# Optimization experiments

Hardware: AMD Instinct MI355X
Metric: run time of the kernel (lower is better)

Reference implementation:

```python
import jax, jax.numpy as jnp
import numpy as np

NUM_TRACKS = [5313, 1643, 128, 0]
MAX_TRACKS = max(NUM_TRACKS)
EMBED_DIM = 1536
LN_EPS = 1e-5


def setup_inputs() -> dict:
    key = jax.random.key(0)
    ks = jax.random.split(key, 8)
    B, S, D = 4, 896, EMBED_DIM
    inp = {
        "x": jax.random.normal(ks[0], (B, S, D), dtype=jnp.float32),
        "head_idx": jax.random.randint(ks[1], (B,), 0, 4, dtype=jnp.int64) if jax.config.jax_enable_x64 else jax.random.randint(ks[1], (B,), 0, 4).astype(jnp.int32),
    }
    for i, n in enumerate([5313, 1643, 128]):
        inp[f"gamma{i}"] = jnp.ones((D,), jnp.float32)
        inp[f"beta{i}"] = jnp.zeros((D,), jnp.float32)
        inp[f"W{i}"] = jax.random.normal(ks[2 + i], (n, D), dtype=jnp.float32) * 0.02
        inp[f"b{i}"] = jnp.zeros((n,), jnp.float32)
    return inp


def _linear_head(x, gamma, beta, W, b):
    # LayerNormFP32 -> Linear -> softplus, cast back to orig dtype
    orig_dtype = x.dtype
    xf = x.astype(jnp.float32)
    mu = jnp.mean(xf, axis=-1, keepdims=True)
    var = jnp.var(xf, axis=-1, keepdims=True)  # biased, as torch LayerNorm
    xn = (xf - mu) * jax.lax.rsqrt(var + LN_EPS) * gamma + beta
    h = jax.nn.softplus(jnp.einsum("bsd,td->bst", xn, W) + b)
    return h.astype(orig_dtype)


def reference(x, head_idx, gamma0, beta0, W0, b0,
              gamma1, beta1, W1, b1, gamma2, beta2, W2, b2):
    params = [(gamma0, beta0, W0, b0),
              (gamma1, beta1, W1, b1),
              (gamma2, beta2, W2, b2),
              None]  # ZeroHead
    B, S, _ = x.shape
    logits = jnp.zeros((B, S, MAX_TRACKS), dtype=x.dtype)
    for i, p in enumerate(params):
        if p is None:
            padded = jnp.zeros((B, S, MAX_TRACKS), dtype=x.dtype)
        else:
            h = _linear_head(x, *p)  # [B, S, n_i]
            pad = MAX_TRACKS - h.shape[-1]
            padded = jnp.pad(h, ((0, 0), (0, 0), (0, pad))) if pad > 0 else h
        mask = (head_idx == i)[:, None, None]
        logits = jnp.where(mask, padded, logits)
    return logits
```

## Files before the change

### kernel.cpp

```cpp
#include <hip/hip_runtime.h>
#include <hip/hip_bf16.h>

#define EMBED 1536
#define SEQ   896
#define NOUT  5313

#define N0 5313
#define N1 1643
#define N2 128
#define W0OFF 0
#define W1OFF 5376
#define W2OFF 7040
#define PTOT  7168

#define LN_BLOCKS 1792
#define WC_BLOCKS 5376
#define GEMM_GRID 1280

typedef __attribute__((ext_vector_type(8))) short bf16x8;
typedef __attribute__((ext_vector_type(4))) float f32x4;

__device__ __forceinline__ void gload_lds16(const void* g, void* l) {
    __builtin_amdgcn_global_load_lds(
        (const __attribute__((address_space(1))) void*)g,
        (__attribute__((address_space(3))) void*)l, 16, 0, 0);
}

__device__ __forceinline__ int tiles_of(int h) {
    return (h == 0) ? 42 : (h == 1) ? 13 : (h == 2) ? 1 : 0;
}
__device__ __forceinline__ int nrows_of(int h) {
    return (h == 0) ? N0 : (h == 1) ? N1 : (h == 2) ? N2 : 0;
}

__global__ __launch_bounds__(256) void prep_kernel(
    const float* __restrict__ x, const int* __restrict__ head_idx,
    const float* __restrict__ g0, const float* __restrict__ be0,
    const float* __restrict__ g1, const float* __restrict__ be1,
    const float* __restrict__ g2, const float* __restrict__ be2,
    const float* __restrict__ W0, const float* __restrict__ W1,
    const float* __restrict__ W2,
    __hip_bfloat16* __restrict__ xn, __hip_bfloat16* __restrict__ wpad)
{
    const int tid = threadIdx.x;

    if (blockIdx.x < LN_BLOCKS) {
        const int half = tid >> 7;
        const int lt   = tid & 127;
        const int row  = blockIdx.x * 2 + half;
        const int b    = row / SEQ;
        const int h    = head_idx[b];
        if (h == 3) return;

        const float* gamma = (h == 1) ? g1 : (h == 2) ? g2 : g0;
        const float* beta  = (h == 1) ? be1 : (h == 2) ? be2 : be0;
        const float* xr = x + (size_t)row * EMBED;

        float4 v[3];
        float sum = 0.f, sq = 0.f;
#pragma unroll
        for (int i = 0; i < 3; ++i) {
            v[i] = ((const float4*)xr)[lt + i * 128];
            sum += v[i].x + v[i].y + v[i].z + v[i].w;
            sq  += v[i].x * v[i].x + v[i].y * v[i].y + v[i].z * v[i].z + v[i].w * v[i].w;
        }
#pragma unroll
        for (int off = 32; off > 0; off >>= 1) {
            sum += __shfl_down(sum, off);
            sq  += __shfl_down(sq, off);
        }
        __shared__ float s_sum[4], s_sq[4];
        const int wave = tid >> 6, lane = tid & 63;
        if (lane == 0) { s_sum[wave] = sum; s_sq[wave] = sq; }
        __syncthreads();
        const int wb = half << 1;
        const float mu  = (s_sum[wb] + s_sum[wb + 1]) * (1.f / EMBED);
        const float var = (s_sq[wb] + s_sq[wb + 1]) * (1.f / EMBED) - mu * mu;
        const float rs  = rsqrtf(var + 1e-5f);

        __hip_bfloat16* xo = xn + (size_t)row * EMBED;
#pragma unroll
        for (int i = 0; i < 3; ++i) {
            const int idx = lt + i * 128;
            float4 gv = ((const float4*)gamma)[idx];
            float4 bv = ((const float4*)beta)[idx];
            union { __hip_bfloat16 h4[4]; short4 s4; } u;
            u.h4[0] = __float2bfloat16((v[i].x - mu) * rs * gv.x + bv.x);
            u.h4[1] = __float2bfloat16((v[i].y - mu) * rs * gv.y + bv.y);
            u.h4[2] = __float2bfloat16((v[i].z - mu) * rs * gv.z + bv.z);
            u.h4[3] = __float2bfloat16((v[i].w - mu) * rs * gv.w + bv.w);
            ((short4*)xo)[idx] = u.s4;
        }
    } else {
        const int gid = (blockIdx.x - LN_BLOCKS) * 256 + tid;
        const int r = gid / 192;
        const int c = (gid - r * 192) * 8;
        const int region = (r < W1OFF) ? 0 : (r < W2OFF) ? 1 : 2;
        const int h0 = head_idx[0], h1 = head_idx[1];
        const int h2 = head_idx[2], h3 = head_idx[3];
        if (region != h0 && region != h1 && region != h2 && region != h3)
            return;
        const float* src = nullptr;
        if (region == 0)      { if (r < N0) src = W0 + (size_t)r * EMBED; }
        else if (region == 1) { int rr = r - W1OFF; if (rr < N1) src = W1 + (size_t)rr * EMBED; }
        else                  { int rr = r - W2OFF; if (rr < N2) src = W2 + (size_t)rr * EMBED; }
        union { __hip_bfloat16 h8[8]; int4 v4; } u;
        if (src) {
            float4 a = ((const float4*)(src + c))[0];
            float4 b = ((const float4*)(src + c))[1];
            u.h8[0] = __float2bfloat16(a.x); u.h8[1] = __float2bfloat16(a.y);
            u.h8[2] = __float2bfloat16(a.z); u.h8[3] = __float2bfloat16(a.w);
            u.h8[4] = __float2bfloat16(b.x); u.h8[5] = __float2bfloat16(b.y);
            u.h8[6] = __float2bfloat16(b.z); u.h8[7] = __float2bfloat16(b.w);
        } else {
            u.v4 = make_int4(0, 0, 0, 0);
        }
        *(int4*)(wpad + (size_t)r * EMBED + c) = u.v4;
    }
}

__global__ __launch_bounds__(256, 2) void head_gemm(
    const __hip_bfloat16* __restrict__ xn,
    const __hip_bfloat16* __restrict__ wpad,
    const float* __restrict__ b0, const float* __restrict__ b1,
    const float* __restrict__ b2,
    const int* __restrict__ head_idx,
    float* __restrict__ out)
{
    const int h0 = head_idx[0], h1 = head_idx[1];
    const int h2 = head_idx[2], h3 = head_idx[3];
    const int t0 = tiles_of(h0) * 7, t1 = tiles_of(h1) * 7;
    const int t2 = tiles_of(h2) * 7, t3 = tiles_of(h3) * 7;
    const int R = t0 + t1 + t2 + t3;
    const int tid = threadIdx.x;

    if ((int)blockIdx.x >= R) {
        const int j = blockIdx.x - R;
        const int ZB = GEMM_GRID - R;
        for (int row = j; row < 4 * SEQ; row += ZB) {
            const int b = row / SEQ;
            const int h = (b == 0) ? h0 : (b == 1) ? h1 : (b == 2) ? h2 : h3;
            const int n = nrows_of(h);
            if (n >= NOUT) continue;
            float* o = out + (size_t)row * NOUT;
            const int pre0 = (4 - (int)(((size_t)row * NOUT + n) & 3)) & 3;
            const int pre_end = min(n + pre0, NOUT);
            for (int c = n + tid; c < pre_end; c += 256) o[c] = 0.f;
            const int nvec = (NOUT - pre_end) >> 2;
            const float4 z = make_float4(0.f, 0.f, 0.f, 0.f);
            float4* ov = (float4*)(o + pre_end);
            for (int i = tid; i < nvec; i += 256) ov[i] = z;
            for (int c = pre_end + (nvec << 2) + tid; c < NOUT; c += 256) o[c] = 0.f;
        }
        return;
    }

    int rem = blockIdx.x, b;
    if (rem < t0)                { b = 0; }
    else if (rem < t0 + t1)      { b = 1; rem -= t0; }
    else if (rem < t0 + t1 + t2) { b = 2; rem -= t0 + t1; }
    else                         { b = 3; rem -= t0 + t1 + t2; }

    const int h = (b == 0) ? h0 : (b == 1) ? h1 : (b == 2) ? h2 : h3;
    const int ntc = tiles_of(h);
    const int mt = rem / ntc;
    const int nt = rem - mt * ntc;
    const int nrows = nrows_of(h);
    const int wbase = (h == 0) ? W0OFF : (h == 1) ? W1OFF : W2OFF;

    const int col0 = nt * 128;
    float* outb = out + ((size_t)b * SEQ + (size_t)mt * 128) * NOUT;

    __shared__ __hip_bfloat16 As[128 * 64];
    __shared__ __hip_bfloat16 Bs[128 * 64];
    const __hip_bfloat16* Ab = xn + ((size_t)b * SEQ + (size_t)mt * 128) * EMBED;
    const __hip_bfloat16* Bb = wpad + (size_t)(wbase + col0) * EMBED;

    const int wave = tid >> 6, lane = tid & 63;
    const int wm = wave >> 1, wn = wave & 1;
    const int fm = lane & 15, quad = lane >> 4;
    const int fsw = fm & 7;

    f32x4 acc[4][4] = {};

    for (int kt = 0; kt < EMBED / 64; ++kt) {
        const int k0 = kt * 64;
        __syncthreads();
#pragma unroll
        for (int i = 0; i < 4; ++i) {
            const int c = tid + i * 256;
            const int arow = c >> 3;
            const int kc = (c & 7) ^ (arow & 7);
            gload_lds16(Ab + (size_t)arow * EMBED + k0 + kc * 8, As + c * 8);
        }
#pragma unroll
        for (int i = 0; i < 4; ++i) {
            const int c = tid + i * 256;
            const int brow = c >> 3;
            const int kc = (c & 7) ^ (brow & 7);
            gload_lds16(Bb + (size_t)brow * EMBED + k0 + kc * 8, Bs + c * 8);
        }
        __syncthreads();
#pragma unroll
        for (int ks = 0; ks < 2; ++ks) {
            bf16x8 af[4], bfr[4];
#pragma unroll
            for (int i = 0; i < 4; ++i)
                af[i] = *(const bf16x8*)&As[(wm * 64 + i * 16 + fm) * 64 +
                                            (((ks << 2) + quad) ^ fsw) * 8];
#pragma unroll
            for (int j = 0; j < 4; ++j)
                bfr[j] = *(const bf16x8*)&Bs[(wn * 64 + j * 16 + fm) * 64 +
                                             (((ks << 2) + quad) ^ fsw) * 8];
#pragma unroll
            for (int i = 0; i < 4; ++i)
#pragma unroll
                for (int j = 0; j < 4; ++j)
                    acc[i][j] = __builtin_amdgcn_mfma_f32_16x16x32_bf16(
                        af[i], bfr[j], acc[i][j], 0, 0, 0);
        }
    }

    const float* bias = (h == 1) ? b1 : (h == 2) ? b2 : b0;
#pragma unroll
    for (int j = 0; j < 4; ++j) {
        const int lcol = col0 + wn * 64 + j * 16 + fm;
        const bool valid = lcol < nrows;
        const float bv = valid ? bias[lcol] : 0.f;
#pragma unroll
        for (int i = 0; i < 4; ++i) {
            const int rbase = wm * 64 + i * 16 + quad * 4;
#pragma unroll
            for (int r = 0; r < 4; ++r) {
                const float v = acc[i][j][r] + bv;
                const float sp = fmaxf(v, 0.f) + __logf(1.f + __expf(-fabsf(v)));
                if (valid) outb[(size_t)(rbase + r) * NOUT + lcol] = sp;
            }
        }
    }
}

extern "C" void kernel_launch(void* const* d_in, const int* in_sizes, int n_in,
                              void* d_out, int out_size, void* d_ws, size_t ws_size,
                              hipStream_t stream) {
    const float* x   = (const float*)d_in[0];
    const int* hidx  = (const int*)d_in[1];
    const float* g0  = (const float*)d_in[2];
    const float* be0 = (const float*)d_in[3];
    const float* W0  = (const float*)d_in[4];
    const float* b0  = (const float*)d_in[5];
    const float* g1  = (const float*)d_in[6];
    const float* be1 = (const float*)d_in[7];
    const float* W1  = (const float*)d_in[8];
    const float* b1  = (const float*)d_in[9];
    const float* g2  = (const float*)d_in[10];
    const float* be2 = (const float*)d_in[11];
    const float* W2  = (const float*)d_in[12];
    const float* b2  = (const float*)d_in[13];
    float* out = (float*)d_out;

    const size_t XN_BYTES = (size_t)4 * SEQ * EMBED * 2;
    __hip_bfloat16* xn   = (__hip_bfloat16*)d_ws;
    __hip_bfloat16* wpad = (__hip_bfloat16*)((char*)d_ws + XN_BYTES);

    prep_kernel<<<LN_BLOCKS + WC_BLOCKS, 256, 0, stream>>>(
        x, hidx, g0, be0, g1, be1, g2, be2, W0, W1, W2, xn, wpad);
    head_gemm<<<GEMM_GRID, 256, 0, stream>>>(xn, wpad, b0, b1, b2, hidx, out);
}
```

Measured before the change: 175.4 us.

## Fuse weight fp32-to-bf16 conversion into GEMM tile loads, drop padded weight buffer

Result: slower. 188.5 us (+7.4%).

```diff
diff --git a/kernel.cpp b/kernel.cpp
--- a/kernel.cpp
+++ b/kernel.cpp
@@ -8,13 +8,8 @@
 #define N0 5313
 #define N1 1643
 #define N2 128
-#define W0OFF 0
-#define W1OFF 5376
-#define W2OFF 7040
-#define PTOT  7168
 
 #define LN_BLOCKS 1792
-#define WC_BLOCKS 5376
 #define GEMM_GRID 1280
 
 typedef __attribute__((ext_vector_type(8))) short bf16x8;
@@ -33,95 +28,66 @@
     return (h == 0) ? N0 : (h == 1) ? N1 : (h == 2) ? N2 : 0;
 }
 
-__global__ __launch_bounds__(256) void prep_kernel(
+__global__ __launch_bounds__(256) void ln_kernel(
     const float* __restrict__ x, const int* __restrict__ head_idx,
     const float* __restrict__ g0, const float* __restrict__ be0,
     const float* __restrict__ g1, const float* __restrict__ be1,
     const float* __restrict__ g2, const float* __restrict__ be2,
+    __hip_bfloat16* __restrict__ xn)
+{
+    const int tid = threadIdx.x;
+    const int half = tid >> 7;
+    const int lt   = tid & 127;
+    const int row  = blockIdx.x * 2 + half;
+    const int b    = row / SEQ;
+    const int h    = head_idx[b];
+    if (h == 3) return;
+
+    const float* gamma = (h == 1) ? g1 : (h == 2) ? g2 : g0;
+    const float* beta  = (h == 1) ? be1 : (h == 2) ? be2 : be0;
+    const float* xr = x + (size_t)row * EMBED;
+
+    float4 v[3];
+    float sum = 0.f, sq = 0.f;
+#pragma unroll
+    for (int i = 0; i < 3; ++i) {
+        v[i] = ((const float4*)xr)[lt + i * 128];
+        sum += v[i].x + v[i].y + v[i].z + v[i].w;
+        sq  += v[i].x * v[i].x + v[i].y * v[i].y + v[i].z * v[i].z + v[i].w * v[i].w;
+    }
+#pragma unroll
+    for (int off = 32; off > 0; off >>= 1) {
+        sum += __shfl_down(sum, off);
+        sq  += __shfl_down(sq, off);
+    }
+    __shared__ float s_sum[4], s_sq[4];
+    const int wave = tid >> 6, lane = tid & 63;
+    if (lane == 0) { s_sum[wave] = sum; s_sq[wave] = sq; }
+    __syncthreads();
+    const int wb = half << 1;
+    const float mu  = (s_sum[wb] + s_sum[wb + 1]) * (1.f / EMBED);
+    const float var = (s_sq[wb] + s_sq[wb + 1]) * (1.f / EMBED) - mu * mu;
+    const float rs  = rsqrtf(var + 1e-5f);
+
+    __hip_bfloat16* xo = xn + (size_t)row * EMBED;
+#pragma unroll
+    for (int i = 0; i < 3; ++i) {
+        const int idx = lt + i * 128;
+        float4 gv = ((const float4*)gamma)[idx];
+        float4 bv = ((const float4*)beta)[idx];
+        union { __hip_bfloat16 h4[4]; short4 s4; } u;
+        u.h4[0] = __float2bfloat16((v[i].x - mu) * rs * gv.x + bv.x);
+        u.h4[1] = __float2bfloat16((v[i].y - mu) * rs * gv.y + bv.y);
+        u.h4[2] = __float2bfloat16((v[i].z - mu) * rs * gv.z + bv.z);
+        u.h4[3] = __float2bfloat16((v[i].w - mu) * rs * gv.w + bv.w);
+        ((short4*)xo)[idx] = u.s4;
+    }
+}
+
+__global__ __launch_bounds__(256, 2) void head_gemm(
+    const __hip_bfloat16* __restrict__ xn,
     const float* __restrict__ W0, const float* __restrict__ W1,
     const float* __restrict__ W2,
-    __hip_bfloat16* __restrict__ xn, __hip_bfloat16* __restrict__ wpad)
-{
-    const int tid = threadIdx.x;
-
-    if (blockIdx.x < LN_BLOCKS) {
-        const int half = tid >> 7;
-        const int lt   = tid & 127;
-        const int row  = blockIdx.x * 2 + half;
-        const int b    = row / SEQ;
-        const int h    = head_idx[b];
-        if (h == 3) return;
-
-        const float* gamma = (h == 1) ? g1 : (h == 2) ? g2 : g0;
-        const float* beta  = (h == 1) ? be1 : (h == 2) ? be2 : be0;
-        const float* xr = x + (size_t)row * EMBED;
-
-        float4 v[3];
-        float sum = 0.f, sq = 0.f;
-#pragma unroll
-        for (int i = 0; i < 3; ++i) {
-            v[i] = ((const float4*)xr)[lt + i * 128];
-            sum += v[i].x + v[i].y + v[i].z + v[i].w;
-            sq  += v[i].x * v[i].x + v[i].y * v[i].y + v[i].z * v[i].z + v[i].w * v[i].w;
-        }
-#pragma unroll
-        for (int off = 32; off > 0; off >>= 1) {
-            sum += __shfl_down(sum, off);
-            sq  += __shfl_down(sq, off);
-        }
-        __shared__ float s_sum[4], s_sq[4];
-        const int wave = tid >> 6, lane = tid & 63;
-        if (lane == 0) { s_sum[wave] = sum; s_sq[wave] = sq; }
-        __syncthreads();
-        const int wb = half << 1;
-        const float mu  = (s_sum[wb] + s_sum[wb + 1]) * (1.f / EMBED);
-        const float var = (s_sq[wb] + s_sq[wb + 1]) * (1.f / EMBED) - mu * mu;
-        const float rs  = rsqrtf(var + 1e-5f);
-
-        __hip_bfloat16* xo = xn + (size_t)row * EMBED;
-#pragma unroll
-        for (int i = 0; i < 3; ++i) {
-            const int idx = lt + i * 128;
-            float4 gv = ((const float4*)gamma)[idx];
-            float4 bv = ((const float4*)beta)[idx];
-            union { __hip_bfloat16 h4[4]; short4 s4; } u;
-            u.h4[0] = __float2bfloat16((v[i].x - mu) * rs * gv.x + bv.x);
-            u.h4[1] = __float2bfloat16((v[i].y - mu) * rs * gv.y + bv.y);
-            u.h4[2] = __float2bfloat16((v[i].z - mu) * rs * gv.z + bv.z);
-            u.h4[3] = __float2bfloat16((v[i].w - mu) * rs * gv.w + bv.w);
-            ((short4*)xo)[idx] = u.s4;
-        }
-    } else {
-        const int gid = (blockIdx.x - LN_BLOCKS) * 256 + tid;
-        const int r = gid / 192;
-        const int c = (gid - r * 192) * 8;
-        const int region = (r < W1OFF) ? 0 : (r < W2OFF) ? 1 : 2;
-        const int h0 = head_idx[0], h1 = head_idx[1];
-        const int h2 = head_idx[2], h3 = head_idx[3];
-        if (region != h0 && region != h1 && region != h2 && region != h3)
-            return;
-        const float* src = nullptr;
-        if (region == 0)      { if (r < N0) src = W0 + (size_t)r * EMBED; }
-        else if (region == 1) { int rr = r - W1OFF; if (rr < N1) src = W1 + (size_t)rr * EMBED; }
-        else                  { int rr = r - W2OFF; if (rr < N2) src = W2 + (size_t)rr * EMBED; }
-        union { __hip_bfloat16 h8[8]; int4 v4; } u;
-        if (src) {
-            float4 a = ((const float4*)(src + c))[0];
-            float4 b = ((const float4*)(src + c))[1];
-            u.h8[0] = __float2bfloat16(a.x); u.h8[1] = __float2bfloat16(a.y);
-            u.h8[2] = __float2bfloat16(a.z); u.h8[3] = __float2bfloat16(a.w);
-            u.h8[4] = __float2bfloat16(b.x); u.h8[5] = __float2bfloat16(b.y);
-            u.h8[6] = __float2bfloat16(b.z); u.h8[7] = __float2bfloat16(b.w);
-        } else {
-            u.v4 = make_int4(0, 0, 0, 0);
-        }
-        *(int4*)(wpad + (size_t)r * EMBED + c) = u.v4;
-    }
-}
-
-__global__ __launch_bounds__(256, 2) void head_gemm(
-    const __hip_bfloat16* __restrict__ xn,
-    const __hip_bfloat16* __restrict__ wpad,
     const float* __restrict__ b0, const float* __restrict__ b1,
     const float* __restrict__ b2,
     const int* __restrict__ head_idx,
@@ -166,7 +132,7 @@
     const int mt = rem / ntc;
     const int nt = rem - mt * ntc;
     const int nrows = nrows_of(h);
-    const int wbase = (h == 0) ? W0OFF : (h == 1) ? W1OFF : W2OFF;
+    const float* __restrict__ Wh = (h == 0) ? W0 : (h == 1) ? W1 : W2;
 
     const int col0 = nt * 128;
     float* outb = out + ((size_t)b * SEQ + (size_t)mt * 128) * NOUT;
@@ -174,12 +140,21 @@
     __shared__ __hip_bfloat16 As[128 * 64];
     __shared__ __hip_bfloat16 Bs[128 * 64];
     const __hip_bfloat16* Ab = xn + ((size_t)b * SEQ + (size_t)mt * 128) * EMBED;
-    const __hip_bfloat16* Bb = wpad + (size_t)(wbase + col0) * EMBED;
 
     const int wave = tid >> 6, lane = tid & 63;
     const int wm = wave >> 1, wn = wave & 1;
     const int fm = lane & 15, quad = lane >> 4;
     const int fsw = fm & 7;
+
+    int bgrow[4], bkc[4], bc[4];
+#pragma unroll
+    for (int i = 0; i < 4; ++i) {
+        const int c = tid + i * 256;
+        const int brow = c >> 3;
+        bkc[i] = (c & 7) ^ (brow & 7);
+        bgrow[i] = min(col0 + brow, nrows - 1);
+        bc[i] = c;
+    }
 
     f32x4 acc[4][4] = {};
 
@@ -195,10 +170,14 @@
         }
 #pragma unroll
         for (int i = 0; i < 4; ++i) {
-            const int c = tid + i * 256;
-            const int brow = c >> 3;
-            const int kc = (c & 7) ^ (brow & 7);
-            gload_lds16(Bb + (size_t)brow * EMBED + k0 + kc * 8, Bs + c * 8);
+            const float4* wp = (const float4*)(Wh + (size_t)bgrow[i] * EMBED + k0 + bkc[i] * 8);
+            float4 a = wp[0], b4 = wp[1];
+            union { __hip_bfloat16 h8[8]; int4 v4; } u;
+            u.h8[0] = __float2bfloat16(a.x);  u.h8[1] = __float2bfloat16(a.y);
+            u.h8[2] = __float2bfloat16(a.z);  u.h8[3] = __float2bfloat16(a.w);
+            u.h8[4] = __float2bfloat16(b4.x); u.h8[5] = __float2bfloat16(b4.y);
+            u.h8[6] = __float2bfloat16(b4.z); u.h8[7] = __float2bfloat16(b4.w);
+            *(int4*)(Bs + bc[i] * 8) = u.v4;
         }
         __syncthreads();
 #pragma unroll
@@ -259,11 +238,10 @@
     const float* b2  = (const float*)d_in[13];
     float* out = (float*)d_out;
 
-    const size_t XN_BYTES = (size_t)4 * SEQ * EMBED * 2;
-    __hip_bfloat16* xn   = (__hip_bfloat16*)d_ws;
-    __hip_bfloat16* wpad = (__hip_bfloat16*)((char*)d_ws + XN_BYTES);
-
-    prep_kernel<<<LN_BLOCKS + WC_BLOCKS, 256, 0, stream>>>(
-        x, hidx, g0, be0, g1, be1, g2, be2, W0, W1, W2, xn, wpad);
-    head_gemm<<<GEMM_GRID, 256, 0, stream>>>(xn, wpad, b0, b1, b2, hidx, out);
-}
+    __hip_bfloat16* xn = (__hip_bfloat16*)d_ws;
+
+    ln_kernel<<<LN_BLOCKS, 256, 0, stream>>>(
+        x, hidx, g0, be0, g1, be1, g2, be2, xn);
+    head_gemm<<<GEMM_GRID, 256, 0, stream>>>(
+        xn, W0, W1, W2, b0, b1, b2, hidx, out);
+}
```

## Double-buffer LDS tiles in GEMM to overlap global loads with MFMA

Applied to the files above, without the earlier changes.

Measured after the change: 176.9 us. Within noise of the previous version (+0.8%).

```diff
diff --git a/kernel.cpp b/kernel.cpp
--- a/kernel.cpp
+++ b/kernel.cpp
@@ -16,6 +16,7 @@
 #define LN_BLOCKS 1792
 #define WC_BLOCKS 5376
 #define GEMM_GRID 1280
+#define BK 64
 
 typedef __attribute__((ext_vector_type(8))) short bf16x8;
 typedef __attribute__((ext_vector_type(4))) float f32x4;
@@ -171,8 +172,8 @@
     const int col0 = nt * 128;
     float* outb = out + ((size_t)b * SEQ + (size_t)mt * 128) * NOUT;
 
-    __shared__ __hip_bfloat16 As[128 * 64];
-    __shared__ __hip_bfloat16 Bs[128 * 64];
+    __shared__ __hip_bfloat16 As[2][128 * BK];
+    __shared__ __hip_bfloat16 Bs[2][128 * BK];
     const __hip_bfloat16* Ab = xn + ((size_t)b * SEQ + (size_t)mt * 128) * EMBED;
     const __hip_bfloat16* Bb = wpad + (size_t)(wbase + col0) * EMBED;
 
@@ -181,37 +182,50 @@
     const int fm = lane & 15, quad = lane >> 4;
     const int fsw = fm & 7;
 
+    const int c0 = tid, c1 = tid + 256, c2 = tid + 512, c3 = tid + 768;
+    const int r0 = c0 >> 3, r1 = c1 >> 3, r2 = c2 >> 3, r3 = c3 >> 3;
+    const int kc0 = (c0 & 7) ^ (r0 & 7), kc1 = (c1 & 7) ^ (r1 & 7);
+    const int kc2 = (c2 & 7) ^ (r2 & 7), kc3 = (c3 & 7) ^ (r3 & 7);
+
     f32x4 acc[4][4] = {};
 
-    for (int kt = 0; kt < EMBED / 64; ++kt) {
-        const int k0 = kt * 64;
+    {
+        gload_lds16(Ab + (size_t)r0 * EMBED + kc0 * 8, &As[0][c0 * 8]);
+        gload_lds16(Ab + (size_t)r1 * EMBED + kc1 * 8, &As[0][c1 * 8]);
+        gload_lds16(Ab + (size_t)r2 * EMBED + kc2 * 8, &As[0][c2 * 8]);
+        gload_lds16(Ab + (size_t)r3 * EMBED + kc3 * 8, &As[0][c3 * 8]);
+        gload_lds16(Bb + (size_t)r0 * EMBED + kc0 * 8, &Bs[0][c0 * 8]);
+        gload_lds16(Bb + (size_t)r1 * EMBED + kc1 * 8, &Bs[0][c1 * 8]);
+        gload_lds16(Bb + (size_t)r2 * EMBED + kc2 * 8, &Bs[0][c2 * 8]);
+        gload_lds16(Bb + (size_t)r3 * EMBED + kc3 * 8, &Bs[0][c3 * 8]);
+    }
+
+    int p = 0;
+    for (int kt = 0; kt < EMBED / BK; ++kt) {
         __syncthreads();
-#pragma unroll
-        for (int i = 0; i < 4; ++i) {
-            const int c = tid + i * 256;
-            const int arow = c >> 3;
-            const int kc = (c & 7) ^ (arow & 7);
-            gload_lds16(Ab + (size_t)arow * EMBED + k0 + kc * 8, As + c * 8);
-        }
-#pragma unroll
-        for (int i = 0; i < 4; ++i) {
-            const int c = tid + i * 256;
-            const int brow = c >> 3;
-            const int kc = (c & 7) ^ (brow & 7);
-            gload_lds16(Bb + (size_t)brow * EMBED + k0 + kc * 8, Bs + c * 8);
-        }
-        __syncthreads();
+        if (kt + 1 < EMBED / BK) {
+            const int kn = (kt + 1) * BK;
+            const int q = p ^ 1;
+            gload_lds16(Ab + (size_t)r0 * EMBED + kn + kc0 * 8, &As[q][c0 * 8]);
+            gload_lds16(Ab + (size_t)r1 * EMBED + kn + kc1 * 8, &As[q][c1 * 8]);
+            gload_lds16(Ab + (size_t)r2 * EMBED + kn + kc2 * 8, &As[q][c2 * 8]);
+            gload_lds16(Ab + (size_t)r3 * EMBED + kn + kc3 * 8, &As[q][c3 * 8]);
+            gload_lds16(Bb + (size_t)r0 * EMBED + kn + kc0 * 8, &Bs[q][c0 * 8]);
+            gload_lds16(Bb + (size_t)r1 * EMBED + kn + kc1 * 8, &Bs[q][c1 * 8]);
+            gload_lds16(Bb + (size_t)r2 * EMBED + kn + kc2 * 8, &Bs[q][c2 * 8]);
+            gload_lds16(Bb + (size_t)r3 * EMBED + kn + kc3 * 8, &Bs[q][c3 * 8]);
+        }
 #pragma unroll
         for (int ks = 0; ks < 2; ++ks) {
             bf16x8 af[4], bfr[4];
 #pragma unroll
             for (int i = 0; i < 4; ++i)
-                af[i] = *(const bf16x8*)&As[(wm * 64 + i * 16 + fm) * 64 +
-                                            (((ks << 2) + quad) ^ fsw) * 8];
+                af[i] = *(const bf16x8*)&As[p][(wm * 64 + i * 16 + fm) * BK +
+                                              (((ks << 2) + quad) ^ fsw) * 8];
 #pragma unroll
             for (int j = 0; j < 4; ++j)
-                bfr[j] = *(const bf16x8*)&Bs[(wn * 64 + j * 16 + fm) * 64 +
-                                             (((ks << 2) + quad) ^ fsw) * 8];
+                bfr[j] = *(const bf16x8*)&Bs[p][(wn * 64 + j * 16 + fm) * BK +
+                                               (((ks << 2) + quad) ^ fsw) * 8];
 #pragma unroll
             for (int i = 0; i < 4; ++i)
 #pragma unroll
@@ -219,6 +233,7 @@
                     acc[i][j] = __builtin_amdgcn_mfma_f32_16x16x32_bf16(
                         af[i], bfr[j], acc[i][j], 0, 0, 0);
         }
+        p ^= 1;
     }
 
     const float* bias = (h == 1) ? b1 : (h == 2) ? b2 : b0;
```
